# Performance work log

Measured on AMD Instinct MI355X. Metric: run time of the kernel, lower is better.

## Reference

```python
import jax, jax.numpy as jnp
import numpy as np

B, C, P, H, W, K = 8, 64, 64, 256, 256, 3
BN_EPS = 1e-5


def setup_inputs() -> dict:
    key = jax.random.key(0)
    k0, k1, k2, k3 = jax.random.split(key, 4)
    x = jax.random.normal(k0, (B, C, H, W), dtype=jnp.float32)
    dw_w = jax.random.normal(k1, (C, K, K), dtype=jnp.float32) * (1.0 / K)
    pw_w = jax.random.normal(k2, (P, C), dtype=jnp.float32) * (1.0 / np.sqrt(C))
    gamma = jnp.ones((P,), dtype=jnp.float32)
    beta = jnp.zeros((P,), dtype=jnp.float32)
    mean = jnp.zeros((P,), dtype=jnp.float32)
    var = jnp.ones((P,), dtype=jnp.float32)
    conv_w = jax.random.normal(k3, (1, P), dtype=jnp.float32) * (1.0 / np.sqrt(P))
    return dict(x=x, dw_w=dw_w, pw_w=pw_w, gamma=gamma, beta=beta,
                mean=mean, var=var, conv_w=conv_w)


def reference(x, dw_w, pw_w, gamma, beta, mean, var, conv_w):
    # Faithful to the torch forward: x[:, i:] = relu6(dw_conv[i](x[:, i:i+1]))
    # broadcasts each 1-channel result over channels i..C-1, so iteration i
    # consumes iteration i-1's output -> a sequential chain seeded by x[:, 0].
    def step(y, w):  # y: [B, H, W], w: [K, K]
        o = jax.lax.conv_general_dilated(
            y[:, None, :, :], w[None, None, :, :],
            window_strides=(1, 1), padding='SAME')[:, 0]
        o = jnp.clip(o, 0.0, 6.0)  # ReLU6
        return o, o

    _, ys = jax.lax.scan(step, x[:, 0], dw_w)      # [C, B, H, W]

    # pointwise conv (1x1, no bias)
    h = jnp.einsum('pc,cbhw->bphw', pw_w, ys)       # [B, P, H, W]

    # BatchNorm (inference form with running stats) + ReLU6
    scale = gamma * jax.lax.rsqrt(var + BN_EPS)
    h = h * scale[None, :, None, None] + (beta - mean * scale)[None, :, None, None]
    h = jnp.clip(h, 0.0, 6.0)

    # final 1x1 conv P -> 1 (no bias)
    out = jnp.einsum('op,bphw->bohw', conv_w, h)    # [B, 1, H, W]
    return out
```

## Files before the change

kernel.cpp:

```cpp
#include <hip/hip_runtime.h>
#include <hip/hip_bf16.h>

#define B_    8
#define C_    64
#define P_    64
#define H_    256
#define W_    256
#define BHW_  (B_ * H_ * W_)
#define BN_EPS 1e-5f

#define CHUNK 16
#define SWC   64

typedef _Float16 half4v __attribute__((ext_vector_type(4)));
typedef _Float16 half8v __attribute__((ext_vector_type(8)));
typedef _Float16 half2v __attribute__((ext_vector_type(2)));
typedef __attribute__((ext_vector_type(4))) float f32x4;

__device__ __forceinline__ float dpp_row_shr1(float v) {
    return __int_as_float(__builtin_amdgcn_update_dpp(
        0, __float_as_int(v), 0x111, 0xF, 0xF, true));
}
__device__ __forceinline__ float dpp_row_shl1(float v) {
    return __int_as_float(__builtin_amdgcn_update_dpp(
        0, __float_as_int(v), 0x101, 0xF, 0xF, true));
}

__global__ __launch_bounds__(1024, 8) void chain_kernel(
    const float* __restrict__ src,
    size_t src_batch_stride,
    const float* __restrict__ dw,
    _Float16* __restrict__ ysh,
    float* __restrict__ seed_out,
    int c0)
{
    __shared__ __align__(16) float buf0[66 * SWC];
    __shared__ __align__(16) float buf1[66 * SWC];
    __shared__ int prog[16];

    const int tid  = threadIdx.x;
    const int w    = tid >> 6;
    const int lane = tid & 63;
    const int row  = tid >> 4;
    const int seg  = tid & 15;
    const int lx   = seg * 4;
    const int b    = blockIdx.z;
    const int ty0  = blockIdx.y * 32;
    const int tx0  = blockIdx.x * 32;
    const int gy   = ty0 - 16 + row;
    const int gx   = tx0 - 16 + lx;
    const bool inImg = (gy >= 0) && (gy < H_) && (gx >= 0) && (gx < W_);
    const float msk = inImg ? 1.0f : 0.0f;
    const int cell = (row + 1) * SWC + lx;

    if (tid < 16) prog[tid] = 0;

    float4 v = make_float4(0.f, 0.f, 0.f, 0.f);
    if (inImg)
        v = *(const float4*)(src + (size_t)b * src_batch_stride
                             + (size_t)gy * W_ + gx);
    *(float4*)&buf0[cell] = v;
    if (row == 0) {
        float4 z = make_float4(0.f, 0.f, 0.f, 0.f);
        *(float4*)&buf0[lx] = z;  *(float4*)&buf0[65 * SWC + lx] = z;
        *(float4*)&buf1[lx] = z;  *(float4*)&buf1[65 * SWC + lx] = z;
    }
    __syncthreads();

    volatile int* vp = prog;
    const int wm1 = (w == 0)  ? 0  : w - 1;
    const int wp1 = (w == 15) ? 15 : w + 1;

    const bool wOK = (row >= 16) && (row < 48) && (seg >= 4) && (seg < 12);
    const size_t goff = (size_t)(b * H_ + gy) * W_ + gx;
    _Float16* gb = ysh + (size_t)c0 * BHW_ + (wOK ? goff : 0);
    float* sb = seed_out ? seed_out + (wOK ? goff : 0) : nullptr;

#pragma unroll
    for (int i = 0; i < CHUNK; ++i) {
        const float w0 = dw[i*9+0], w1 = dw[i*9+1], w2 = dw[i*9+2];
        const float w3 = dw[i*9+3], w4 = dw[i*9+4], w5 = dw[i*9+5];
        const float w6 = dw[i*9+6], w7 = dw[i*9+7], w8 = dw[i*9+8];

        while (vp[wm1] < i || vp[wp1] < i) {  }

        float* cur = (i & 1) ? buf1 : buf0;
        float* nxt = (i & 1) ? buf0 : buf1;

        float4 rT = *(const float4*)&cur[cell - SWC];
        float4 rM = *(const float4*)&cur[cell];
        float4 rB = *(const float4*)&cur[cell + SWC];

        float tl = dpp_row_shr1(rT.w), tr = dpp_row_shl1(rT.x);
        float ml = dpp_row_shr1(rM.w), mr = dpp_row_shl1(rM.x);
        float bl = dpp_row_shr1(rB.w), br = dpp_row_shl1(rB.x);

        float s0 = fmaf(tl,   w0, fmaf(rT.x, w1, fmaf(rT.y, w2,
                   fmaf(ml,   w3, fmaf(rM.x, w4, fmaf(rM.y, w5,
                   fmaf(bl,   w6, fmaf(rB.x, w7, rB.y * w8))))))));
        float s1 = fmaf(rT.x, w0, fmaf(rT.y, w1, fmaf(rT.z, w2,
                   fmaf(rM.x, w3, fmaf(rM.y, w4, fmaf(rM.z, w5,
                   fmaf(rB.x, w6, fmaf(rB.y, w7, rB.z * w8))))))));
        float s2 = fmaf(rT.y, w0, fmaf(rT.z, w1, fmaf(rT.w, w2,
                   fmaf(rM.y, w3, fmaf(rM.z, w4, fmaf(rM.w, w5,
                   fmaf(rB.y, w6, fmaf(rB.z, w7, rB.w * w8))))))));
        float s3 = fmaf(rT.z, w0, fmaf(rT.w, w1, fmaf(tr,   w2,
                   fmaf(rM.z, w3, fmaf(rM.w, w4, fmaf(mr,   w5,
                   fmaf(rB.z, w6, fmaf(rB.w, w7, br   * w8))))))));
        float4 ov;
        ov.x = fminf(fmaxf(s0, 0.f), 6.f) * msk;
        ov.y = fminf(fmaxf(s1, 0.f), 6.f) * msk;
        ov.z = fminf(fmaxf(s2, 0.f), 6.f) * msk;
        ov.w = fminf(fmaxf(s3, 0.f), 6.f) * msk;

        if (i < CHUNK - 1) {
            *(float4*)&nxt[cell] = ov;
            __threadfence_block();
            if (lane == 0) vp[w] = i + 1;
        }

        if (wOK) {
            half4v hv;
            hv.x = (_Float16)ov.x; hv.y = (_Float16)ov.y;
            hv.z = (_Float16)ov.z; hv.w = (_Float16)ov.w;
            *(half4v*)(gb + (size_t)i * BHW_) = hv;
            if (i == CHUNK - 1 && sb)
                *(float4*)sb = ov;
        }
    }
}

__global__ __launch_bounds__(256) void fuse_mfma(
    const _Float16* __restrict__ ysh,
    const float* __restrict__ pw_w,
    const float* __restrict__ gamma,
    const float* __restrict__ beta,
    const float* __restrict__ mean,
    const float* __restrict__ var,
    const float* __restrict__ conv_w,
    float* __restrict__ out)
{
    __shared__ _Float16 yt[64 * 88];
    __shared__ float2 bc[P_];

    const int tid  = threadIdx.x;
    const int lane = tid & 63;
    const int wv   = tid >> 6;
    const int nIdx = lane & 15;
    const int quad = lane >> 4;

    if (tid < P_) {
        float sc = gamma[tid] * rsqrtf(var[tid] + BN_EPS);
        bc[tid] = make_float2(beta[tid] - mean[tid] * sc, conv_w[tid]);
    }

    half8v Ah[4][2], Al[4][2];
#pragma unroll
    for (int pt = 0; pt < 4; ++pt) {
        const int p = pt * 16 + nIdx;
        const float sc = gamma[p] * rsqrtf(var[p] + BN_EPS);
#pragma unroll
        for (int kt = 0; kt < 2; ++kt) {
            const float* ap = pw_w + p * C_ + kt * 32 + quad * 8;
            half8v hh, ll;
#pragma unroll
            for (int j = 0; j < 8; ++j) {
                float a = ap[j] * sc;
                _Float16 h = (_Float16)a;
                hh[j] = h;
                ll[j] = (_Float16)(a - (float)h);
            }
            Ah[pt][kt] = hh;
            Al[pt][kt] = ll;
        }
    }
    __syncthreads();

    const int px2 = (tid & 31) * 2;
    const int c8  = (tid >> 5) * 8;

    for (int tile = blockIdx.x; tile < BHW_ / 64; tile += gridDim.x) {
        const size_t base = (size_t)tile * 64;

        half2v yv[8];
#pragma unroll
        for (int j = 0; j < 8; ++j)
            yv[j] = *(const half2v*)(ysh + (size_t)(c8 + j) * BHW_ + base + px2);

        __syncthreads();

        half8v e0, e1;
#pragma unroll
        for (int j = 0; j < 8; ++j) { e0[j] = yv[j].x; e1[j] = yv[j].y; }
        *(half8v*)&yt[px2 * 88 + c8]       = e0;
        *(half8v*)&yt[(px2 + 1) * 88 + c8] = e1;

        __syncthreads();

        f32x4 acc[4];
#pragma unroll
        for (int pt = 0; pt < 4; ++pt) acc[pt] = (f32x4){0.f, 0.f, 0.f, 0.f};

        const int col = wv * 16 + nIdx;
#pragma unroll
        for (int kt = 0; kt < 2; ++kt) {
            half8v Bv = *(half8v*)&yt[col * 88 + kt * 32 + quad * 8];
#pragma unroll
            for (int pt = 0; pt < 4; ++pt) {
                acc[pt] = __builtin_amdgcn_mfma_f32_16x16x32_f16(
                    Ah[pt][kt], Bv, acc[pt], 0, 0, 0);
                acc[pt] = __builtin_amdgcn_mfma_f32_16x16x32_f16(
                    Al[pt][kt], Bv, acc[pt], 0, 0, 0);
            }
        }

        float sum = 0.f;
#pragma unroll
        for (int pt = 0; pt < 4; ++pt) {
#pragma unroll
            for (int r = 0; r < 4; ++r) {
                const int p = pt * 16 + quad * 4 + r;
                float2 bcv = bc[p];
                float vv = fminf(fmaxf(acc[pt][r] + bcv.x, 0.f), 6.f);
                sum = fmaf(bcv.y, vv, sum);
            }
        }
        sum += __shfl_xor(sum, 16, 64);
        sum += __shfl_xor(sum, 32, 64);
        if (lane < 16)
            out[base + wv * 16 + lane] = sum;
    }
}

extern "C" void kernel_launch(void* const* d_in, const int* in_sizes, int n_in,
                              void* d_out, int out_size, void* d_ws, size_t ws_size,
                              hipStream_t stream) {
    const float* x      = (const float*)d_in[0];
    const float* dw_w   = (const float*)d_in[1];
    const float* pw_w   = (const float*)d_in[2];
    const float* gamma  = (const float*)d_in[3];
    const float* beta   = (const float*)d_in[4];
    const float* mean   = (const float*)d_in[5];
    const float* var    = (const float*)d_in[6];
    const float* conv_w = (const float*)d_in[7];
    float* out = (float*)d_out;

    _Float16* ysh = (_Float16*)d_ws;
    float* seeds = (float*)((char*)d_ws + (size_t)C_ * BHW_ * sizeof(_Float16));

    dim3 cgrid(W_ / 32, H_ / 32, B_);

    chain_kernel<<<cgrid, 1024, 0, stream>>>(
        x, (size_t)C_ * H_ * W_, dw_w, ysh, seeds, 0);
    for (int k = 1; k < C_ / CHUNK; ++k) {
        float* seed_out = (k < 3) ? seeds + (size_t)k * BHW_ : nullptr;
        chain_kernel<<<cgrid, 1024, 0, stream>>>(
            seeds + (size_t)(k - 1) * BHW_, (size_t)H_ * W_,
            dw_w + k * CHUNK * 9, ysh, seed_out, k * CHUNK);
    }

    fuse_mfma<<<1024, 256, 0, stream>>>(
        ysh, pw_w, gamma, beta, mean, var, conv_w, out);
}
```

Baseline: 270.8 us.

## Double-buffer LDS tile and prefetch next tile in fused pointwise kernel

Switches the fused pointwise/BN/conv kernel to a double-buffered shared-memory tile and issues the global loads for the next tile before computing the current one. This drops one barrier per iteration and overlaps the fp16 activation reads with the MFMA work. The grid also grows from 1024 to 2048 blocks, and the prefetch stride is tied to that block count. The cost is more LDS per block and more live registers for the prefetched values, which may reduce occupancy.

```diff
diff --git a/kernel.cpp b/kernel.cpp
--- a/kernel.cpp
+++ b/kernel.cpp
@@ -11,6 +11,7 @@
 
 #define CHUNK 16
 #define SWC   64
+#define FT_BLOCKS 2048
 
 typedef _Float16 half4v __attribute__((ext_vector_type(4)));
 typedef _Float16 half8v __attribute__((ext_vector_type(8)));
@@ -140,7 +141,7 @@
     const float* __restrict__ conv_w,
     float* __restrict__ out)
 {
-    __shared__ _Float16 yt[64 * 88];
+    __shared__ _Float16 yt[2][64 * 88];
     __shared__ float2 bc[P_];
 
     const int tid  = threadIdx.x;
@@ -174,37 +175,48 @@
             Al[pt][kt] = ll;
         }
     }
-    __syncthreads();
 
     const int px2 = (tid & 31) * 2;
     const int c8  = (tid >> 5) * 8;
-
-    for (int tile = blockIdx.x; tile < BHW_ / 64; tile += gridDim.x) {
-        const size_t base = (size_t)tile * 64;
-
-        half2v yv[8];
-#pragma unroll
-        for (int j = 0; j < 8; ++j)
-            yv[j] = *(const half2v*)(ysh + (size_t)(c8 + j) * BHW_ + base + px2);
+    const int col = wv * 16 + nIdx;
+
+    const int nTiles = BHW_ / 64;
+    int tile = blockIdx.x;
+
+    half2v yv[8];
+#pragma unroll
+    for (int j = 0; j < 8; ++j)
+        yv[j] = *(const half2v*)(ysh + (size_t)(c8 + j) * BHW_
+                                 + (size_t)tile * 64 + px2);
+
+    __syncthreads();
+
+    for (int iter = 0; tile < nTiles; ++iter) {
+        _Float16* buf = yt[iter & 1];
+
+        half8v e0, e1;
+#pragma unroll
+        for (int j = 0; j < 8; ++j) { e0[j] = yv[j].x; e1[j] = yv[j].y; }
+        *(half8v*)&buf[px2 * 88 + c8]       = e0;
+        *(half8v*)&buf[(px2 + 1) * 88 + c8] = e1;
+
+        const int next = tile + FT_BLOCKS;
+        if (next < nTiles) {
+#pragma unroll
+            for (int j = 0; j < 8; ++j)
+                yv[j] = *(const half2v*)(ysh + (size_t)(c8 + j) * BHW_
+                                         + (size_t)next * 64 + px2);
+        }
 
         __syncthreads();
 
-        half8v e0, e1;
-#pragma unroll
-        for (int j = 0; j < 8; ++j) { e0[j] = yv[j].x; e1[j] = yv[j].y; }
-        *(half8v*)&yt[px2 * 88 + c8]       = e0;
-        *(half8v*)&yt[(px2 + 1) * 88 + c8] = e1;
-
-        __syncthreads();
-
         f32x4 acc[4];
 #pragma unroll
         for (int pt = 0; pt < 4; ++pt) acc[pt] = (f32x4){0.f, 0.f, 0.f, 0.f};
 
-        const int col = wv * 16 + nIdx;
 #pragma unroll
         for (int kt = 0; kt < 2; ++kt) {
-            half8v Bv = *(half8v*)&yt[col * 88 + kt * 32 + quad * 8];
+            half8v Bv = *(half8v*)&buf[col * 88 + kt * 32 + quad * 8];
 #pragma unroll
             for (int pt = 0; pt < 4; ++pt) {
                 acc[pt] = __builtin_amdgcn_mfma_f32_16x16x32_f16(
@@ -228,7 +240,9 @@
         sum += __shfl_xor(sum, 16, 64);
         sum += __shfl_xor(sum, 32, 64);
         if (lane < 16)
-            out[base + wv * 16 + lane] = sum;
+            out[(size_t)tile * 64 + wv * 16 + lane] = sum;
+
+        tile = next;
     }
 }
 
@@ -259,6 +273,6 @@
             dw_w + k * CHUNK * 9, ysh, seed_out, k * CHUNK);
     }
 
-    fuse_mfma<<<1024, 256, 0, stream>>>(
+    fuse_mfma<<<FT_BLOCKS, 256, 0, stream>>>(
         ysh, pw_w, gamma, beta, mean, var, conv_w, out);
 }
```

Result: no change. 267.7 us (-1.2%).
